# Kernel tuning notes

Measured on AMD Instinct MI355X. Metric: run time of the kernel, lower is better.

The kernel has to match this reference:

```python
import jax, jax.numpy as jnp
import numpy as np

MARGIN = 0.5  # forward body overrides self.margin = 0.5 inside the loop


def setup_inputs() -> dict:
    key = jax.random.key(0)
    k1, k2 = jax.random.split(key)
    B, H, W = 8, 64, 64
    pred_weights = jax.random.normal(k1, (B, H, W), dtype=jnp.float32)
    true_mask = jax.random.uniform(k2, (B, H, W), dtype=jnp.float32)
    return {"pred_weights": pred_weights, "true_mask": true_mask}


def reference(pred_weights, true_mask):
    B = pred_weights.shape[0]
    x = pred_weights.reshape(B, -1)          # [B, N], N = H*W
    m = true_mask.reshape(B, -1)
    # per-sample max normalization (torch.max over flattened sample)
    x = x / jnp.max(x, axis=1, keepdims=True)
    pos_m = (m > 0.5).astype(x.dtype)        # [B, N]
    neg_m = (m < 0.5).astype(x.dtype)
    # masked pairwise margin: relu(margin - (pos_i - neg_j)) over pos x neg pairs
    diff = MARGIN - (x[:, :, None] - x[:, None, :])  # [B, N, N]
    w = pos_m[:, :, None] * neg_m[:, None, :]        # pair validity mask
    per_sample = jnp.sum(jax.nn.relu(diff) * w, axis=(1, 2))  # [B]
    n_pos = jnp.sum(pos_m, axis=1)
    n_neg = jnp.sum(neg_m, axis=1)
    denom = n_pos * n_neg + 1e-8
    valid = (n_pos > 0) & (n_neg > 0)        # skip samples with empty pos/neg
    sample_loss = jnp.where(valid, per_sample / denom, 0.0)
    # reduction == 'mean' divides by batch size
    return jnp.sum(sample_loss) / B
```

## Files before the change

### kernel.cpp

```cpp
#include <hip/hip_runtime.h>

#define BATCH 8
#define N 4096
#define TPB 512
#define SPB 32
#define NBLK (BATCH * SPB)
#define POS_F 4096
#define SENT_NEG -1.0e30f
#define SENT_POS  1.0e30f

__global__ __launch_bounds__(TPB) void srs_fused_kernel(
    const float* __restrict__ pred,
    const float* __restrict__ mask,
    float* __restrict__ out,
    float* __restrict__ partials,
    unsigned int* __restrict__ cnt)
{
    const int b    = blockIdx.x >> 5;
    const int c    = blockIdx.x & 31;
    const int tid  = threadIdx.x;
    const int lane = tid & 63;
    const int wid  = tid >> 6;

    __shared__ float4 comb4[2048];
    float* comb = (float*)comb4;
    __shared__ float red[8];
    __shared__ int ctr[2];

    const float4* xb4 = (const float4*)(pred + b * N);
    const float4* mb4 = (const float4*)(mask + b * N);

    float4 xv0 = xb4[tid];
    float4 xv1 = xb4[tid + 512];
    float4 mv0 = mb4[tid];
    float4 mv1 = mb4[tid + 512];

    comb4[tid]        = make_float4(SENT_NEG, SENT_NEG, SENT_NEG, SENT_NEG);
    comb4[tid + 512]  = make_float4(SENT_NEG, SENT_NEG, SENT_NEG, SENT_NEG);
    comb4[tid + 1024] = make_float4(SENT_POS, SENT_POS, SENT_POS, SENT_POS);
    comb4[tid + 1536] = make_float4(SENT_POS, SENT_POS, SENT_POS, SENT_POS);
    if (tid < 2) ctr[tid] = 0;

    float lmax = fmaxf(fmaxf(xv0.x, xv0.y), fmaxf(xv0.z, xv0.w));
    lmax = fmaxf(lmax, fmaxf(fmaxf(xv1.x, xv1.y), fmaxf(xv1.z, xv1.w)));
    for (int off = 32; off > 0; off >>= 1)
        lmax = fmaxf(lmax, __shfl_down(lmax, off));
    if (lane == 0) red[wid] = lmax;
    __syncthreads();

    float mx = red[0];
#pragma unroll
    for (int w = 1; w < 8; ++w) mx = fmaxf(mx, red[w]);
    const float rmax = 1.0f / mx;

    float xs[8] = {xv0.x, xv0.y, xv0.z, xv0.w, xv1.x, xv1.y, xv1.z, xv1.w};
    float ms[8] = {mv0.x, mv0.y, mv0.z, mv0.w, mv1.x, mv1.y, mv1.z, mv1.w};
    bool isp[8], isn[8];
    unsigned long long bp[8], bn[8];
#pragma unroll
    for (int k = 0; k < 8; ++k) {
        isp[k] = ms[k] > 0.5f;
        isn[k] = ms[k] < 0.5f;
        bp[k] = __ballot(isp[k]);
        bn[k] = __ballot(isn[k]);
    }
    int cp = 0, cn = 0;
#pragma unroll
    for (int k = 0; k < 8; ++k) { cp += (int)__popcll(bp[k]); cn += (int)__popcll(bn[k]); }
    int basep = 0, basen = 0;
    if (lane == 0) {
        basep = atomicAdd(&ctr[0], cp);
        basen = atomicAdd(&ctr[1], cn);
    }
    basep = __shfl(basep, 0);
    basen = __shfl(basen, 0);
    const unsigned long long lower = (1ull << lane) - 1ull;
    int op = 0, on = 0;
#pragma unroll
    for (int k = 0; k < 8; ++k) {
        float nv = xs[k] * rmax;
        if (isp[k]) comb[POS_F + basep + op + (int)__popcll(bp[k] & lower)] = nv;
        if (isn[k]) comb[basen + on + (int)__popcll(bn[k] & lower)] = nv + 0.5f;
        op += (int)__popcll(bp[k]);
        on += (int)__popcll(bn[k]);
    }
    __syncthreads();

    const int npos = ctr[0], nneg = ctr[1];
    const int ii = tid & 31;
    const int jsplit = tid >> 5;
    float a0=0.f,a1=0.f,a2=0.f,a3=0.f,a4=0.f,a5=0.f,a6=0.f,a7=0.f;

    if (npos <= nneg) {
        const float xiA = comb[POS_F + c * 64 + ii];
        const float xiB = comb[POS_F + c * 64 + ii + 32];
        const int nj4 = (nneg + 3) >> 2;
#pragma unroll 2
        for (int j4 = jsplit; j4 < nj4; j4 += 16) {
            float4 v = comb4[j4];
            a0 += fmaxf(v.x - xiA, 0.f); a1 += fmaxf(v.y - xiA, 0.f);
            a2 += fmaxf(v.z - xiA, 0.f); a3 += fmaxf(v.w - xiA, 0.f);
            a4 += fmaxf(v.x - xiB, 0.f); a5 += fmaxf(v.y - xiB, 0.f);
            a6 += fmaxf(v.z - xiB, 0.f); a7 += fmaxf(v.w - xiB, 0.f);
        }
    } else {
        const float wjA = comb[c * 64 + ii];
        const float wjB = comb[c * 64 + ii + 32];
        const int nj4 = (npos + 3) >> 2;
#pragma unroll 2
        for (int j4 = jsplit; j4 < nj4; j4 += 16) {
            float4 v = comb4[1024 + j4];
            a0 += fmaxf(wjA - v.x, 0.f); a1 += fmaxf(wjA - v.y, 0.f);
            a2 += fmaxf(wjA - v.z, 0.f); a3 += fmaxf(wjA - v.w, 0.f);
            a4 += fmaxf(wjB - v.x, 0.f); a5 += fmaxf(wjB - v.y, 0.f);
            a6 += fmaxf(wjB - v.z, 0.f); a7 += fmaxf(wjB - v.w, 0.f);
        }
    }
    float acc = ((a0 + a1) + (a2 + a3)) + ((a4 + a5) + (a6 + a7));
    for (int off = 32; off > 0; off >>= 1) acc += __shfl_down(acc, off);
    if (lane == 0) red[wid] = acc;
    __syncthreads();

    if (wid == 0) {
        float tot = 0.f;
#pragma unroll
        for (int w = 0; w < 8; ++w) tot += red[w];
        const float denom = (float)npos * (float)nneg + 1e-8f;
        const float scale = (npos > 0 && nneg > 0) ? 1.0f / (denom * (float)BATCH) : 0.0f;
        const float part = tot * scale;
        int last = 0;
        if (lane == 0) {
            __hip_atomic_store(&partials[blockIdx.x], part,
                               __ATOMIC_RELEASE, __HIP_MEMORY_SCOPE_AGENT);
            unsigned int old = __hip_atomic_fetch_add(cnt, 1u, __ATOMIC_ACQ_REL,
                                                      __HIP_MEMORY_SCOPE_AGENT);
            last = (((old + 1u) & (NBLK - 1u)) == 0u) ? 1 : 0;
        }
        last = __shfl(last, 0);
        if (last) {
            float s = 0.f;
#pragma unroll
            for (int k = 0; k < NBLK / 64; ++k)
                s += __hip_atomic_load(&partials[lane + 64 * k],
                                       __ATOMIC_RELAXED, __HIP_MEMORY_SCOPE_AGENT);
            for (int off = 32; off > 0; off >>= 1) s += __shfl_down(s, off);
            if (lane == 0)
                __hip_atomic_store(out, s, __ATOMIC_RELEASE, __HIP_MEMORY_SCOPE_AGENT);
        }
    }
}

extern "C" void kernel_launch(void* const* d_in, const int* in_sizes, int n_in,
                              void* d_out, int out_size, void* d_ws, size_t ws_size,
                              hipStream_t stream) {
    const float* pred = (const float*)d_in[0];
    const float* mask = (const float*)d_in[1];
    float* out = (float*)d_out;
    float* partials = (float*)d_ws;
    unsigned int* cnt = (unsigned int*)((char*)d_ws + NBLK * sizeof(float));

    srs_fused_kernel<<<NBLK, TPB, 0, stream>>>(pred, mask, out, partials, cnt);
}
```

Before: 17.48 us.

## Merge max and count barriers, defer normalization, widen per-thread register tile

Removes one block barrier by publishing the per-wave max together with per-wave pos/neg counts, then computing the prefix offsets from shared memory instead of LDS atomics. Stores raw values and folds the max normalization into a bias of 0.5*max plus a final rmax scale. This relies on relu(m - d/mx) = relu(m*mx - d)/mx, which holds only when mx is positive. Each thread now handles 4 outer elements against strided inner chunks (16 accumulators) instead of 2, which halves shared-memory reads per pair at the cost of more registers.

```diff
diff --git a/kernel.cpp b/kernel.cpp
--- a/kernel.cpp
+++ b/kernel.cpp
@@ -25,7 +25,7 @@
     __shared__ float4 comb4[2048];
     float* comb = (float*)comb4;
     __shared__ float red[8];
-    __shared__ int ctr[2];
+    __shared__ int wcp[8], wcn[8];
 
     const float4* xb4 = (const float4*)(pred + b * N);
     const float4* mb4 = (const float4*)(mask + b * N);
@@ -39,19 +39,6 @@
     comb4[tid + 512]  = make_float4(SENT_NEG, SENT_NEG, SENT_NEG, SENT_NEG);
     comb4[tid + 1024] = make_float4(SENT_POS, SENT_POS, SENT_POS, SENT_POS);
     comb4[tid + 1536] = make_float4(SENT_POS, SENT_POS, SENT_POS, SENT_POS);
-    if (tid < 2) ctr[tid] = 0;
-
-    float lmax = fmaxf(fmaxf(xv0.x, xv0.y), fmaxf(xv0.z, xv0.w));
-    lmax = fmaxf(lmax, fmaxf(fmaxf(xv1.x, xv1.y), fmaxf(xv1.z, xv1.w)));
-    for (int off = 32; off > 0; off >>= 1)
-        lmax = fmaxf(lmax, __shfl_down(lmax, off));
-    if (lane == 0) red[wid] = lmax;
-    __syncthreads();
-
-    float mx = red[0];
-#pragma unroll
-    for (int w = 1; w < 8; ++w) mx = fmaxf(mx, red[w]);
-    const float rmax = 1.0f / mx;
 
     float xs[8] = {xv0.x, xv0.y, xv0.z, xv0.w, xv1.x, xv1.y, xv1.z, xv1.w};
     float ms[8] = {mv0.x, mv0.y, mv0.z, mv0.w, mv1.x, mv1.y, mv1.z, mv1.w};
@@ -67,56 +54,87 @@
     int cp = 0, cn = 0;
 #pragma unroll
     for (int k = 0; k < 8; ++k) { cp += (int)__popcll(bp[k]); cn += (int)__popcll(bn[k]); }
+
+    float lmax = fmaxf(fmaxf(xs[0], xs[1]), fmaxf(xs[2], xs[3]));
+    lmax = fmaxf(lmax, fmaxf(fmaxf(xs[4], xs[5]), fmaxf(xs[6], xs[7])));
+    for (int off = 32; off > 0; off >>= 1)
+        lmax = fmaxf(lmax, __shfl_down(lmax, off));
+    if (lane == 0) { red[wid] = lmax; wcp[wid] = cp; wcn[wid] = cn; }
+    __syncthreads();
+
+    float mx = red[0];
     int basep = 0, basen = 0;
-    if (lane == 0) {
-        basep = atomicAdd(&ctr[0], cp);
-        basen = atomicAdd(&ctr[1], cn);
+#pragma unroll
+    for (int w = 1; w < 8; ++w) mx = fmaxf(mx, red[w]);
+#pragma unroll
+    for (int w = 0; w < 8; ++w) {
+        if (w < wid) { basep += wcp[w]; basen += wcn[w]; }
     }
-    basep = __shfl(basep, 0);
-    basen = __shfl(basen, 0);
+    const float rmax = 1.0f / mx;
+    const float bias = 0.5f * mx;
+
     const unsigned long long lower = (1ull << lane) - 1ull;
-    int op = 0, on = 0;
 #pragma unroll
     for (int k = 0; k < 8; ++k) {
-        float nv = xs[k] * rmax;
-        if (isp[k]) comb[POS_F + basep + op + (int)__popcll(bp[k] & lower)] = nv;
-        if (isn[k]) comb[basen + on + (int)__popcll(bn[k] & lower)] = nv + 0.5f;
-        op += (int)__popcll(bp[k]);
-        on += (int)__popcll(bn[k]);
+        if (isp[k]) comb[POS_F + basep + (int)__popcll(bp[k] & lower)] = xs[k];
+        if (isn[k]) comb[basen + (int)__popcll(bn[k] & lower)] = xs[k];
+        basep += (int)__popcll(bp[k]);
+        basen += (int)__popcll(bn[k]);
     }
     __syncthreads();
 
-    const int npos = ctr[0], nneg = ctr[1];
-    const int ii = tid & 31;
-    const int jsplit = tid >> 5;
-    float a0=0.f,a1=0.f,a2=0.f,a3=0.f,a4=0.f,a5=0.f,a6=0.f,a7=0.f;
+    int npos = 0, nneg = 0;
+#pragma unroll
+    for (int w = 0; w < 8; ++w) { npos += wcp[w]; nneg += wcn[w]; }
+
+    const int ii = tid & 15;
+    const int jsplit = tid >> 4;
+    float a[16];
+#pragma unroll
+    for (int q = 0; q < 16; ++q) a[q] = 0.f;
 
     if (npos <= nneg) {
-        const float xiA = comb[POS_F + c * 64 + ii];
-        const float xiB = comb[POS_F + c * 64 + ii + 32];
+        const int obase = POS_F + c * 64 + ii;
+        float xi0 = comb[obase]      - bias;
+        float xi1 = comb[obase + 16] - bias;
+        float xi2 = comb[obase + 32] - bias;
+        float xi3 = comb[obase + 48] - bias;
         const int nj4 = (nneg + 3) >> 2;
 #pragma unroll 2
-        for (int j4 = jsplit; j4 < nj4; j4 += 16) {
+        for (int j4 = jsplit; j4 < nj4; j4 += 32) {
             float4 v = comb4[j4];
-            a0 += fmaxf(v.x - xiA, 0.f); a1 += fmaxf(v.y - xiA, 0.f);
-            a2 += fmaxf(v.z - xiA, 0.f); a3 += fmaxf(v.w - xiA, 0.f);
-            a4 += fmaxf(v.x - xiB, 0.f); a5 += fmaxf(v.y - xiB, 0.f);
-            a6 += fmaxf(v.z - xiB, 0.f); a7 += fmaxf(v.w - xiB, 0.f);
+            a[0]  += fmaxf(v.x - xi0, 0.f); a[1]  += fmaxf(v.y - xi0, 0.f);
+            a[2]  += fmaxf(v.z - xi0, 0.f); a[3]  += fmaxf(v.w - xi0, 0.f);
+            a[4]  += fmaxf(v.x - xi1, 0.f); a[5]  += fmaxf(v.y - xi1, 0.f);
+            a[6]  += fmaxf(v.z - xi1, 0.f); a[7]  += fmaxf(v.w - xi1, 0.f);
+            a[8]  += fmaxf(v.x - xi2, 0.f); a[9]  += fmaxf(v.y - xi2, 0.f);
+            a[10] += fmaxf(v.z - xi2, 0.f); a[11] += fmaxf(v.w - xi2, 0.f);
+            a[12] += fmaxf(v.x - xi3, 0.f); a[13] += fmaxf(v.y - xi3, 0.f);
+            a[14] += fmaxf(v.z - xi3, 0.f); a[15] += fmaxf(v.w - xi3, 0.f);
         }
     } else {
-        const float wjA = comb[c * 64 + ii];
-        const float wjB = comb[c * 64 + ii + 32];
+        const int obase = c * 64 + ii;
+        float wj0 = comb[obase]      + bias;
+        float wj1 = comb[obase + 16] + bias;
+        float wj2 = comb[obase + 32] + bias;
+        float wj3 = comb[obase + 48] + bias;
         const int nj4 = (npos + 3) >> 2;
 #pragma unroll 2
-        for (int j4 = jsplit; j4 < nj4; j4 += 16) {
+        for (int j4 = jsplit; j4 < nj4; j4 += 32) {
             float4 v = comb4[1024 + j4];
-            a0 += fmaxf(wjA - v.x, 0.f); a1 += fmaxf(wjA - v.y, 0.f);
-            a2 += fmaxf(wjA - v.z, 0.f); a3 += fmaxf(wjA - v.w, 0.f);
-            a4 += fmaxf(wjB - v.x, 0.f); a5 += fmaxf(wjB - v.y, 0.f);
-            a6 += fmaxf(wjB - v.z, 0.f); a7 += fmaxf(wjB - v.w, 0.f);
+            a[0]  += fmaxf(wj0 - v.x, 0.f); a[1]  += fmaxf(wj0 - v.y, 0.f);
+            a[2]  += fmaxf(wj0 - v.z, 0.f); a[3]  += fmaxf(wj0 - v.w, 0.f);
+            a[4]  += fmaxf(wj1 - v.x, 0.f); a[5]  += fmaxf(wj1 - v.y, 0.f);
+            a[6]  += fmaxf(wj1 - v.z, 0.f); a[7]  += fmaxf(wj1 - v.w, 0.f);
+            a[8]  += fmaxf(wj2 - v.x, 0.f); a[9]  += fmaxf(wj2 - v.y, 0.f);
+            a[10] += fmaxf(wj2 - v.z, 0.f); a[11] += fmaxf(wj2 - v.w, 0.f);
+            a[12] += fmaxf(wj3 - v.x, 0.f); a[13] += fmaxf(wj3 - v.y, 0.f);
+            a[14] += fmaxf(wj3 - v.z, 0.f); a[15] += fmaxf(wj3 - v.w, 0.f);
         }
     }
-    float acc = ((a0 + a1) + (a2 + a3)) + ((a4 + a5) + (a6 + a7));
+    float acc = 0.f;
+#pragma unroll
+    for (int q = 0; q < 16; ++q) acc += a[q];
     for (int off = 32; off > 0; off >>= 1) acc += __shfl_down(acc, off);
     if (lane == 0) red[wid] = acc;
     __syncthreads();
@@ -126,7 +144,8 @@
 #pragma unroll
         for (int w = 0; w < 8; ++w) tot += red[w];
         const float denom = (float)npos * (float)nneg + 1e-8f;
-        const float scale = (npos > 0 && nneg > 0) ? 1.0f / (denom * (float)BATCH) : 0.0f;
+        const float scale = (npos > 0 && nneg > 0)
+                          ? rmax / (denom * (float)BATCH) : 0.0f;
         const float part = tot * scale;
         int last = 0;
         if (lane == 0) {
```

New measurement: 17.08 us. 1.02x faster.
